# Kernel optimization log

Hardware: AMD Instinct MI355X
Metric: run time of the kernel (lower is better)

The kernel has to match this reference:

```python
import jax, jax.numpy as jnp
import numpy as np

N_HEADS = 16

def setup_inputs() -> dict:
    key = jax.random.key(0)
    ks = jax.random.split(key, 8)
    bs, t, h, dh = 32, 512, 1024, 64
    s = lambda k, shape: jax.random.normal(k, shape, dtype=jnp.float32) * 0.02
    return {
        "x": jax.random.normal(ks[0], (bs, t, h), dtype=jnp.float32),
        "Wq": s(ks[1], (h, h)),
        "bq": s(ks[2], (h,)),
        "Wk": s(ks[3], (h, h)),
        "bk": s(ks[4], (h,)),
        "Wv": s(ks[5], (h, dh)),
        "bv": s(ks[6], (dh,)),
        "Wo": s(ks[7], (dh, h)),
    }

def reference(x, Wq, bq, Wk, bk, Wv, bv, Wo):
    bs, t, h = x.shape
    dh = Wv.shape[1]
    nh = N_HEADS
    # projections (context == x; static_features=None path)
    q = (x @ Wq + bq).reshape(bs, t, nh, dh)   # [b,t,h,d]
    k = (x @ Wk + bk).reshape(bs, t, nh, dh)
    v = x @ Wv + bv                             # shared single-head V: [b,t,d]
    scale = dh ** -0.5
    # per-head scores [b,h,q,k]
    score = jnp.einsum('bqhd,bkhd->bhqk', q, k) * scale
    # causal mask (mask_future_timesteps=True): -inf above diagonal
    mask = jnp.triu(jnp.full((t, t), -jnp.inf, dtype=score.dtype), 1)
    score = score + mask
    prob = jax.nn.softmax(score, axis=-1)       # attn_dropout is identity (p=0)
    # broadcast shared V across heads
    attn_vec = jnp.einsum('bhqk,bkd->bhqd', prob, v)   # [b,h,t,d]
    m_attn_vec = jnp.mean(attn_vec, axis=1)            # head-mean pooling [b,t,d]
    out = m_attn_vec @ Wo                              # out_proj, no bias; out_dropout identity
    return out, attn_vec
```

## Files before the change

### kernel.cpp

```cpp
#include <hip/hip_runtime.h>
#include <hip/hip_bf16.h>
#include <math.h>

#define BS 32
#define TT 512
#define HH 1024
#define NH 16
#define DH 64
#define MM (BS*TT)
#define NCAT 2176

typedef __attribute__((ext_vector_type(8))) __bf16 bf16x8;
typedef __attribute__((ext_vector_type(4))) float  f32x4;

#define QSCALE 0.18033688011112042f

__device__ __forceinline__ void gld16(const void* g, void* l) {
    __builtin_amdgcn_global_load_lds(
        (const __attribute__((address_space(1))) unsigned int*)g,
        (__attribute__((address_space(3))) unsigned int*)l,
        16, 0, 0);
}

__global__ __launch_bounds__(256) void cvt_x(const float* __restrict__ x,
                                             __bf16* __restrict__ xb)
{
    const size_t i = ((size_t)blockIdx.x * 256 + threadIdx.x) * 8;
    float4 a = *(const float4*)(x + i);
    float4 b = *(const float4*)(x + i + 4);
    bf16x8 v;
    v[0] = (__bf16)a.x; v[1] = (__bf16)a.y; v[2] = (__bf16)a.z; v[3] = (__bf16)a.w;
    v[4] = (__bf16)b.x; v[5] = (__bf16)b.y; v[6] = (__bf16)b.z; v[7] = (__bf16)b.w;
    *(bf16x8*)(xb + i) = v;
}

__global__ __launch_bounds__(256) void prep_w(
    const float* __restrict__ Wq, const float* __restrict__ Wk,
    const float* __restrict__ Wv, const float* __restrict__ bq_,
    const float* __restrict__ bk_, const float* __restrict__ bv_,
    __bf16* __restrict__ Wt, float* __restrict__ bias_cat)
{
    __shared__ __align__(16) __bf16 tile[64][72];
    const int tid = threadIdx.x;
    const int n0 = blockIdx.x * 64;
    const int k0 = blockIdx.y * 64;

    const int n_l = tid & 63;
    const int k_b = tid >> 6;
    const int n   = n0 + n_l;
    #pragma unroll
    for (int j = 0; j < 16; ++j) {
        const int k_l = j * 4 + k_b;
        const int k   = k0 + k_l;
        float v;
        if (n < 1024)      v = Wq[(size_t)k * 1024 + n];
        else if (n < 2048) v = Wk[(size_t)k * 1024 + (n - 1024)];
        else if (n < 2112) v = Wv[(size_t)k * 64 + (n - 2048)];
        else               v = 0.f;
        tile[n_l][k_l] = (__bf16)v;
    }
    if (blockIdx.y == 0 && tid < 64) {
        const int nn = n0 + tid;
        bias_cat[nn] = (nn < 1024) ? bq_[nn]
                     : (nn < 2048) ? bk_[nn - 1024]
                     : (nn < 2112) ? bv_[nn - 2048] : 0.f;
    }
    __syncthreads();
    const int n_l2 = tid >> 2;
    const int k_l2 = (tid & 3) * 16;
    __bf16* dst = Wt + (size_t)(n0 + n_l2) * 1024 + k0 + k_l2;
    *(bf16x8*)dst       = *(const bf16x8*)&tile[n_l2][k_l2];
    *(bf16x8*)(dst + 8) = *(const bf16x8*)&tile[n_l2][k_l2 + 8];
}

__global__ __launch_bounds__(256) void gemm_qkv(
    const __bf16* __restrict__ A, const __bf16* __restrict__ B,
    const float* __restrict__ bias_cat,
    __bf16* __restrict__ Qo, __bf16* __restrict__ Ko,
    __bf16* __restrict__ Vt)
{
    __shared__ __align__(16) __bf16 sA[128 * 32];
    __shared__ __align__(16) __bf16 sB[128 * 32];

    const int tid  = threadIdx.x;
    const int wv   = tid >> 6;
    const int ln   = tid & 63;
    const int quad = ln >> 4;
    const int l16  = ln & 15;
    const int m0 = blockIdx.y * 128;
    const int n0 = blockIdx.x * 128;

    const int rw = (wv & 1) * 64;
    const int cw = (wv >> 1) * 64;

    f32x4 acc[4][4];
    #pragma unroll
    for (int i = 0; i < 4; ++i)
        #pragma unroll
        for (int j = 0; j < 4; ++j) acc[i][j] = f32x4{0, 0, 0, 0};

    const int srow = wv * 16 + (ln >> 2);
    const int scol = (ln & 3) * 8;
    const __bf16* ga0 = A + (size_t)(m0 + srow) * 1024 + scol;
    const __bf16* gb0 = B + (size_t)(n0 + srow) * 1024 + scol;
    __bf16* la0 = sA + wv * 512;
    __bf16* lb0 = sB + wv * 512;

    for (int k0 = 0; k0 < 1024; k0 += 32) {
        gld16(ga0 + k0, la0);
        gld16(ga0 + (size_t)64 * 1024 + k0, la0 + 2048);
        gld16(gb0 + k0, lb0);
        gld16(gb0 + (size_t)64 * 1024 + k0, lb0 + 2048);
        __syncthreads();

        bf16x8 af[4], bfr[4];
        #pragma unroll
        for (int mt = 0; mt < 4; ++mt)
            af[mt] = *(const bf16x8*)&sA[(rw + mt * 16 + l16) * 32 + quad * 8];
        #pragma unroll
        for (int nt = 0; nt < 4; ++nt)
            bfr[nt] = *(const bf16x8*)&sB[(cw + nt * 16 + l16) * 32 + quad * 8];
        #pragma unroll
        for (int mt = 0; mt < 4; ++mt)
            #pragma unroll
            for (int nt = 0; nt < 4; ++nt)
                acc[mt][nt] = __builtin_amdgcn_mfma_f32_16x16x32_bf16(af[mt], bfr[nt], acc[mt][nt], 0, 0, 0);
        __syncthreads();
    }

    #pragma unroll
    for (int mt = 0; mt < 4; ++mt) {
        #pragma unroll
        for (int nt = 0; nt < 4; ++nt) {
            const int colb = n0 + cw + nt * 16 + l16;
            if (colb >= 2112) continue;
            const float bias = bias_cat[colb];
            #pragma unroll
            for (int r = 0; r < 4; ++r) {
                const int row = m0 + rw + mt * 16 + quad * 4 + r;
                const int b = row >> 9, t = row & 511;
                float v = acc[mt][nt][r] + bias;
                if (colb < 1024) {
                    const int h = colb >> 6, d = colb & 63;
                    Qo[(((size_t)(b * NH + h) * TT) + t) * DH + d] = (__bf16)(v * QSCALE);
                } else if (colb < 2048) {
                    const int c = colb - 1024;
                    const int h = c >> 6, d = c & 63;
                    Ko[(((size_t)(b * NH + h) * TT) + t) * DH + d] = (__bf16)v;
                } else {
                    const int d = colb - 2048;
                    Vt[((size_t)(b * DH + d)) * TT + t] = (__bf16)v;
                }
            }
        }
    }
}

__global__ __launch_bounds__(1024) void attn_mfma(
    const __bf16* __restrict__ Q, const __bf16* __restrict__ K,
    const __bf16* __restrict__ Vt, float* __restrict__ attn_vec,
    float* __restrict__ mav)
{
    __shared__ float smav[64][65];

    const int wave = threadIdx.x >> 6;
    const int lane = threadIdx.x & 63;
    const int pair = blockIdx.x & 7;
    const int b    = blockIdx.x >> 3;
    const int bh   = b * NH + wave;
    const int quad = lane >> 4;
    const int l16  = lane & 15;

    {
        float* p = &smav[0][0];
        for (int i = threadIdx.x; i < 64 * 65; i += 1024) p[i] = 0.f;
    }
    __syncthreads();

    const __bf16* Qbh = Q  + (size_t)bh * TT * DH;
    const __bf16* Kbh = K  + (size_t)bh * TT * DH;
    const __bf16* Vb  = Vt + (size_t)b  * DH * TT;

    const int perm = ((l16 >> 2) << 3) + (l16 & 3);
    const __bf16* kp1 = Kbh + (size_t)perm * DH;
    const __bf16* kp2 = Kbh + (size_t)(perm + 4) * DH;

    #pragma unroll 1
    for (int rep = 0; rep < 2; ++rep) {
        const int qt2 = rep ? (15 - pair) : pair;
        const int q0  = qt2 << 5;
        const int kend = q0 + 32;

        const bf16x8 qA_lo = *(const bf16x8*)(Qbh + (size_t)(q0 + l16) * DH + quad * 8);
        const bf16x8 qA_hi = *(const bf16x8*)(Qbh + (size_t)(q0 + l16) * DH + 32 + quad * 8);
        const bf16x8 qB_lo = *(const bf16x8*)(Qbh + (size_t)(q0 + 16 + l16) * DH + quad * 8);
        const bf16x8 qB_hi = *(const bf16x8*)(Qbh + (size_t)(q0 + 16 + l16) * DH + 32 + quad * 8);

        f32x4 OA[4] = {f32x4{0,0,0,0}, f32x4{0,0,0,0}, f32x4{0,0,0,0}, f32x4{0,0,0,0}};
        f32x4 OB[4] = {f32x4{0,0,0,0}, f32x4{0,0,0,0}, f32x4{0,0,0,0}, f32x4{0,0,0,0}};
        float lA = 0.f, lB = 0.f;

        bf16x8 k1a = *(const bf16x8*)(kp1 + quad * 8);
        bf16x8 k1b = *(const bf16x8*)(kp1 + 32 + quad * 8);
        bf16x8 k2a = *(const bf16x8*)(kp2 + quad * 8);
        bf16x8 k2b = *(const bf16x8*)(kp2 + 32 + quad * 8);

        for (int kb0 = 0; kb0 < kend; kb0 += 32) {
            const __bf16* vp = Vb + (size_t)l16 * TT + kb0 + quad * 8;
            bf16x8 vf0 = *(const bf16x8*)(vp);
            bf16x8 vf1 = *(const bf16x8*)(vp + (size_t)16 * TT);
            bf16x8 vf2 = *(const bf16x8*)(vp + (size_t)32 * TT);
            bf16x8 vf3 = *(const bf16x8*)(vp + (size_t)48 * TT);

            f32x4 s1A = __builtin_amdgcn_mfma_f32_16x16x32_bf16(k1a, qA_lo, f32x4{0,0,0,0}, 0, 0, 0);
            s1A       = __builtin_amdgcn_mfma_f32_16x16x32_bf16(k1b, qA_hi, s1A, 0, 0, 0);
            f32x4 s2A = __builtin_amdgcn_mfma_f32_16x16x32_bf16(k2a, qA_lo, f32x4{0,0,0,0}, 0, 0, 0);
            s2A       = __builtin_amdgcn_mfma_f32_16x16x32_bf16(k2b, qA_hi, s2A, 0, 0, 0);
            f32x4 s1B = __builtin_amdgcn_mfma_f32_16x16x32_bf16(k1a, qB_lo, f32x4{0,0,0,0}, 0, 0, 0);
            s1B       = __builtin_amdgcn_mfma_f32_16x16x32_bf16(k1b, qB_hi, s1B, 0, 0, 0);
            f32x4 s2B = __builtin_amdgcn_mfma_f32_16x16x32_bf16(k2a, qB_lo, f32x4{0,0,0,0}, 0, 0, 0);
            s2B       = __builtin_amdgcn_mfma_f32_16x16x32_bf16(k2b, qB_hi, s2B, 0, 0, 0);

            {
                const int kbn = (kb0 + 32 < kend) ? kb0 + 32 : kb0;
                const __bf16* nk1 = kp1 + (size_t)kbn * DH;
                const __bf16* nk2 = kp2 + (size_t)kbn * DH;
                k1a = *(const bf16x8*)(nk1 + quad * 8);
                k1b = *(const bf16x8*)(nk1 + 32 + quad * 8);
                k2a = *(const bf16x8*)(nk2 + quad * 8);
                k2b = *(const bf16x8*)(nk2 + 32 + quad * 8);
            }

            if (kb0 == q0) {
                const int qqA = q0 + l16, qqB = q0 + 16 + l16;
                #pragma unroll
                for (int r = 0; r < 4; ++r) {
                    const int key1 = kb0 + quad * 8 + r;
                    const int key2 = key1 + 4;
                    if (key1 > qqA) s1A[r] = -INFINITY;
                    if (key2 > qqA) s2A[r] = -INFINITY;
                    if (key1 > qqB) s1B[r] = -INFINITY;
                    if (key2 > qqB) s2B[r] = -INFINITY;
                }
            }

            bf16x8 pfA, pfB;
            float psA = 0.f, psB = 0.f;
            #pragma unroll
            for (int r = 0; r < 4; ++r) {
                float pa0 = exp2f(s1A[r]);
                float pa1 = exp2f(s2A[r]);
                float pb0 = exp2f(s1B[r]);
                float pb1 = exp2f(s2B[r]);
                psA += pa0 + pa1;
                psB += pb0 + pb1;
                pfA[r]     = (__bf16)pa0;
                pfA[4 + r] = (__bf16)pa1;
                pfB[r]     = (__bf16)pb0;
                pfB[4 + r] = (__bf16)pb1;
            }
            lA += psA;
            lB += psB;

            OA[0] = __builtin_amdgcn_mfma_f32_16x16x32_bf16(pfA, vf0, OA[0], 0, 0, 0);
            OB[0] = __builtin_amdgcn_mfma_f32_16x16x32_bf16(pfB, vf0, OB[0], 0, 0, 0);
            OA[1] = __builtin_amdgcn_mfma_f32_16x16x32_bf16(pfA, vf1, OA[1], 0, 0, 0);
            OB[1] = __builtin_amdgcn_mfma_f32_16x16x32_bf16(pfB, vf1, OB[1], 0, 0, 0);
            OA[2] = __builtin_amdgcn_mfma_f32_16x16x32_bf16(pfA, vf2, OA[2], 0, 0, 0);
            OB[2] = __builtin_amdgcn_mfma_f32_16x16x32_bf16(pfB, vf2, OB[2], 0, 0, 0);
            OA[3] = __builtin_amdgcn_mfma_f32_16x16x32_bf16(pfA, vf3, OA[3], 0, 0, 0);
            OB[3] = __builtin_amdgcn_mfma_f32_16x16x32_bf16(pfB, vf3, OB[3], 0, 0, 0);
        }

        lA += __shfl_xor(lA, 16);
        lA += __shfl_xor(lA, 32);
        lB += __shfl_xor(lB, 16);
        lB += __shfl_xor(lB, 32);

        #pragma unroll
        for (int r = 0; r < 4; ++r) {
            const float invA = 1.0f / __shfl(lA, quad * 4 + r);
            const float invB = 1.0f / __shfl(lB, quad * 4 + r);
            const int tA = q0 + quad * 4 + r;
            const int tB = tA + 16;
            const int ltA = rep * 32 + quad * 4 + r;
            const int ltB = ltA + 16;
            float* opA = attn_vec + ((size_t)bh * TT + tA) * DH + l16;
            float* opB = attn_vec + ((size_t)bh * TT + tB) * DH + l16;
            #pragma unroll
            for (int nt = 0; nt < 4; ++nt) {
                const float vA = OA[nt][r] * invA;
                const float vB = OB[nt][r] * invB;
                opA[nt * 16] = vA;
                opB[nt * 16] = vB;
                atomicAdd(&smav[ltA][nt * 16 + l16], vA * (1.f / 16.f));
                atomicAdd(&smav[ltB][nt * 16 + l16], vB * (1.f / 16.f));
            }
        }
    }

    __syncthreads();

    {
        const int row = threadIdx.x >> 4;
        const int d0  = (threadIdx.x & 15) * 4;
        const int t   = (row < 32) ? ((pair << 5) + row)
                                   : (((15 - pair) << 5) + (row - 32));
        float4 v;
        v.x = smav[row][d0];
        v.y = smav[row][d0 + 1];
        v.z = smav[row][d0 + 2];
        v.w = smav[row][d0 + 3];
        *(float4*)(mav + ((size_t)(b * TT + t)) * DH + d0) = v;
    }
}

__global__ __launch_bounds__(256) void gemm_out(
    const float* __restrict__ A, const float* __restrict__ B,
    float* __restrict__ C, int M, int N, int K)
{
    __shared__ __align__(16) __bf16 sA[64][32];
    __shared__ __align__(16) __bf16 sB[64][32];

    const int tid  = threadIdx.x;
    const int wave = tid >> 6;
    const int lane = tid & 63;
    const int m0 = blockIdx.y * 64;
    const int n0 = blockIdx.x * 64;

    f32x4 acc[4] = {f32x4{0,0,0,0}, f32x4{0,0,0,0}, f32x4{0,0,0,0}, f32x4{0,0,0,0}};

    const int ar = tid >> 2;
    const int ac = (tid & 3) * 8;
    const int bk = tid >> 3;
    const int bc = (tid & 7) * 8;
    const int quad = lane >> 4;
    const int l16  = lane & 15;

    for (int k0 = 0; k0 < K; k0 += 32) {
        const float* ap = A + (size_t)(m0 + ar) * K + k0 + ac;
        float4 a0 = *(const float4*)ap;
        float4 a1 = *(const float4*)(ap + 4);
        {
            bf16x8 av;
            av[0] = (__bf16)a0.x; av[1] = (__bf16)a0.y; av[2] = (__bf16)a0.z; av[3] = (__bf16)a0.w;
            av[4] = (__bf16)a1.x; av[5] = (__bf16)a1.y; av[6] = (__bf16)a1.z; av[7] = (__bf16)a1.w;
            *(bf16x8*)&sA[ar][ac] = av;
        }
        const float* bp = B + (size_t)(k0 + bk) * N + n0 + bc;
        float4 b0 = *(const float4*)bp;
        float4 b1 = *(const float4*)(bp + 4);
        sB[bc + 0][bk] = (__bf16)b0.x;
        sB[bc + 1][bk] = (__bf16)b0.y;
        sB[bc + 2][bk] = (__bf16)b0.z;
        sB[bc + 3][bk] = (__bf16)b0.w;
        sB[bc + 4][bk] = (__bf16)b1.x;
        sB[bc + 5][bk] = (__bf16)b1.y;
        sB[bc + 6][bk] = (__bf16)b1.z;
        sB[bc + 7][bk] = (__bf16)b1.w;
        __syncthreads();

        bf16x8 afrag = *(const bf16x8*)&sA[wave * 16 + l16][quad * 8];
        #pragma unroll
        for (int tn = 0; tn < 4; ++tn) {
            bf16x8 bfrag = *(const bf16x8*)&sB[tn * 16 + l16][quad * 8];
            acc[tn] = __builtin_amdgcn_mfma_f32_16x16x32_bf16(afrag, bfrag, acc[tn], 0, 0, 0);
        }
        __syncthreads();
    }

    #pragma unroll
    for (int tn = 0; tn < 4; ++tn) {
        #pragma unroll
        for (int r = 0; r < 4; ++r) {
            int row = m0 + wave * 16 + quad * 4 + r;
            int col = n0 + tn * 16 + l16;
            C[(size_t)row * N + col] = acc[tn][r];
        }
    }
}

extern "C" void kernel_launch(void* const* d_in, const int* in_sizes, int n_in,
                              void* d_out, int out_size, void* d_ws, size_t ws_size,
                              hipStream_t stream)
{
    const float* x  = (const float*)d_in[0];
    const float* Wq = (const float*)d_in[1];
    const float* bq = (const float*)d_in[2];
    const float* Wk = (const float*)d_in[3];
    const float* bk = (const float*)d_in[4];
    const float* Wv = (const float*)d_in[5];
    const float* bv = (const float*)d_in[6];
    const float* Wo = (const float*)d_in[7];

    float* out      = (float*)d_out;
    float* attn_vec = out + (size_t)MM * HH;

    char* ws = (char*)d_ws;
    __bf16* xb  = (__bf16*)ws;
    __bf16* Wt  = xb + (size_t)MM * HH;
    float* bias_cat = (float*)(Wt + (size_t)NCAT * HH);
    __bf16* Qb  = (__bf16*)(bias_cat + 2304);
    __bf16* Kb  = Qb + (size_t)MM * HH;
    __bf16* Vt  = Kb + (size_t)MM * HH;
    float*  mav = (float*)xb;

    cvt_x<<<MM * HH / (256 * 8), 256, 0, stream>>>(x, xb);
    prep_w<<<dim3(NCAT / 64, HH / 64), 256, 0, stream>>>(Wq, Wk, Wv, bq, bk, bv, Wt, bias_cat);
    gemm_qkv<<<dim3(NCAT / 128, MM / 128), 256, 0, stream>>>(xb, Wt, bias_cat, Qb, Kb, Vt);
    attn_mfma<<<BS * 8, 1024, 0, stream>>>(Qb, Kb, Vt, attn_vec, mav);
    gemm_out<<<dim3(HH / 64, MM / 64), 256, 0, stream>>>(mav, Wo, out, MM, HH, DH);
}
```

Before: 436.6 us.

## Stage V in LDS, double-prefetch K, and swizzle QKV GEMM block order

The attention kernel now loads the whole per-batch transposed V tile (64x512 bf16) into shared memory once per block with global_load_lds, replacing repeated global V loads inside the key loop. The K-fragment prefetch becomes two-deep so loads are issued a full iteration earlier. Separately, the QKV GEMM remaps block indices with a swizzle meant to improve L2 locality across the 17-column grid. This costs about 66KB more LDS per block and more registers, which may limit occupancy.

```diff
diff --git a/kernel.cpp b/kernel.cpp
--- a/kernel.cpp
+++ b/kernel.cpp
@@ -87,8 +87,11 @@
     const int ln   = tid & 63;
     const int quad = ln >> 4;
     const int l16  = ln & 15;
-    const int m0 = blockIdx.y * 128;
-    const int n0 = blockIdx.x * 128;
+
+    const int orig = blockIdx.y * 17 + blockIdx.x;
+    const int swz  = (orig & 7) * 272 + (orig >> 3);
+    const int m0 = (swz / 17) * 128;
+    const int n0 = (swz % 17) * 128;
 
     const int rw = (wv & 1) * 64;
     const int cw = (wv >> 1) * 64;
@@ -161,6 +164,7 @@
     const __bf16* __restrict__ Vt, float* __restrict__ attn_vec,
     float* __restrict__ mav)
 {
+    __shared__ __align__(16) __bf16 sV[64][520];
     __shared__ float smav[64][65];
 
     const int wave = threadIdx.x >> 6;
@@ -175,15 +179,22 @@
         float* p = &smav[0][0];
         for (int i = threadIdx.x; i < 64 * 65; i += 1024) p[i] = 0.f;
     }
-    __syncthreads();
-
-    const __bf16* Qbh = Q  + (size_t)bh * TT * DH;
-    const __bf16* Kbh = K  + (size_t)bh * TT * DH;
-    const __bf16* Vb  = Vt + (size_t)b  * DH * TT;
+
+    const __bf16* Vb = Vt + (size_t)b * DH * TT;
+    #pragma unroll
+    for (int r = 0; r < 4; ++r) {
+        const int row = wave + r * 16;
+        gld16(Vb + (size_t)row * TT + lane * 8, &sV[row][0]);
+    }
+
+    const __bf16* Qbh = Q + (size_t)bh * TT * DH;
+    const __bf16* Kbh = K + (size_t)bh * TT * DH;
 
     const int perm = ((l16 >> 2) << 3) + (l16 & 3);
     const __bf16* kp1 = Kbh + (size_t)perm * DH;
     const __bf16* kp2 = Kbh + (size_t)(perm + 4) * DH;
+
+    __syncthreads();
 
     #pragma unroll 1
     for (int rep = 0; rep < 2; ++rep) {
@@ -200,36 +211,31 @@
         f32x4 OB[4] = {f32x4{0,0,0,0}, f32x4{0,0,0,0}, f32x4{0,0,0,0}, f32x4{0,0,0,0}};
         float lA = 0.f, lB = 0.f;
 
-        bf16x8 k1a = *(const bf16x8*)(kp1 + quad * 8);
-        bf16x8 k1b = *(const bf16x8*)(kp1 + 32 + quad * 8);
-        bf16x8 k2a = *(const bf16x8*)(kp2 + quad * 8);
-        bf16x8 k2b = *(const bf16x8*)(kp2 + 32 + quad * 8);
+        bf16x8 c1a = *(const bf16x8*)(kp1 + quad * 8);
+        bf16x8 c1b = *(const bf16x8*)(kp1 + 32 + quad * 8);
+        bf16x8 c2a = *(const bf16x8*)(kp2 + quad * 8);
+        bf16x8 c2b = *(const bf16x8*)(kp2 + 32 + quad * 8);
+        const int kb1 = (32 < kend) ? 32 : 0;
+        bf16x8 n1a = *(const bf16x8*)(kp1 + (size_t)kb1 * DH + quad * 8);
+        bf16x8 n1b = *(const bf16x8*)(kp1 + (size_t)kb1 * DH + 32 + quad * 8);
+        bf16x8 n2a = *(const bf16x8*)(kp2 + (size_t)kb1 * DH + quad * 8);
+        bf16x8 n2b = *(const bf16x8*)(kp2 + (size_t)kb1 * DH + 32 + quad * 8);
 
         for (int kb0 = 0; kb0 < kend; kb0 += 32) {
-            const __bf16* vp = Vb + (size_t)l16 * TT + kb0 + quad * 8;
-            bf16x8 vf0 = *(const bf16x8*)(vp);
-            bf16x8 vf1 = *(const bf16x8*)(vp + (size_t)16 * TT);
-            bf16x8 vf2 = *(const bf16x8*)(vp + (size_t)32 * TT);
-            bf16x8 vf3 = *(const bf16x8*)(vp + (size_t)48 * TT);
-
-            f32x4 s1A = __builtin_amdgcn_mfma_f32_16x16x32_bf16(k1a, qA_lo, f32x4{0,0,0,0}, 0, 0, 0);
-            s1A       = __builtin_amdgcn_mfma_f32_16x16x32_bf16(k1b, qA_hi, s1A, 0, 0, 0);
-            f32x4 s2A = __builtin_amdgcn_mfma_f32_16x16x32_bf16(k2a, qA_lo, f32x4{0,0,0,0}, 0, 0, 0);
-            s2A       = __builtin_amdgcn_mfma_f32_16x16x32_bf16(k2b, qA_hi, s2A, 0, 0, 0);
-            f32x4 s1B = __builtin_amdgcn_mfma_f32_16x16x32_bf16(k1a, qB_lo, f32x4{0,0,0,0}, 0, 0, 0);
-            s1B       = __builtin_amdgcn_mfma_f32_16x16x32_bf16(k1b, qB_hi, s1B, 0, 0, 0);
-            f32x4 s2B = __builtin_amdgcn_mfma_f32_16x16x32_bf16(k2a, qB_lo, f32x4{0,0,0,0}, 0, 0, 0);
-            s2B       = __builtin_amdgcn_mfma_f32_16x16x32_bf16(k2b, qB_hi, s2B, 0, 0, 0);
-
-            {
-                const int kbn = (kb0 + 32 < kend) ? kb0 + 32 : kb0;
-                const __bf16* nk1 = kp1 + (size_t)kbn * DH;
-                const __bf16* nk2 = kp2 + (size_t)kbn * DH;
-                k1a = *(const bf16x8*)(nk1 + quad * 8);
-                k1b = *(const bf16x8*)(nk1 + 32 + quad * 8);
-                k2a = *(const bf16x8*)(nk2 + quad * 8);
-                k2b = *(const bf16x8*)(nk2 + 32 + quad * 8);
-            }
+            const int vcol = kb0 + quad * 8;
+            bf16x8 vf0 = *(const bf16x8*)&sV[l16][vcol];
+            bf16x8 vf1 = *(const bf16x8*)&sV[16 + l16][vcol];
+            bf16x8 vf2 = *(const bf16x8*)&sV[32 + l16][vcol];
+            bf16x8 vf3 = *(const bf16x8*)&sV[48 + l16][vcol];
+
+            f32x4 s1A = __builtin_amdgcn_mfma_f32_16x16x32_bf16(c1a, qA_lo, f32x4{0,0,0,0}, 0, 0, 0);
+            s1A       = __builtin_amdgcn_mfma_f32_16x16x32_bf16(c1b, qA_hi, s1A, 0, 0, 0);
+            f32x4 s2A = __builtin_amdgcn_mfma_f32_16x16x32_bf16(c2a, qA_lo, f32x4{0,0,0,0}, 0, 0, 0);
+            s2A       = __builtin_amdgcn_mfma_f32_16x16x32_bf16(c2b, qA_hi, s2A, 0, 0, 0);
+            f32x4 s1B = __builtin_amdgcn_mfma_f32_16x16x32_bf16(c1a, qB_lo, f32x4{0,0,0,0}, 0, 0, 0);
+            s1B       = __builtin_amdgcn_mfma_f32_16x16x32_bf16(c1b, qB_hi, s1B, 0, 0, 0);
+            f32x4 s2B = __builtin_amdgcn_mfma_f32_16x16x32_bf16(c2a, qB_lo, f32x4{0,0,0,0}, 0, 0, 0);
+            s2B       = __builtin_amdgcn_mfma_f32_16x16x32_bf16(c2b, qB_hi, s2B, 0, 0, 0);
 
             if (kb0 == q0) {
                 const int qqA = q0 + l16, qqB = q0 + 16 + l16;
@@ -270,6 +276,15 @@
             OB[2] = __builtin_amdgcn_mfma_f32_16x16x32_bf16(pfB, vf2, OB[2], 0, 0, 0);
             OA[3] = __builtin_amdgcn_mfma_f32_16x16x32_bf16(pfA, vf3, OA[3], 0, 0, 0);
             OB[3] = __builtin_amdgcn_mfma_f32_16x16x32_bf16(pfB, vf3, OB[3], 0, 0, 0);
+
+            c1a = n1a; c1b = n1b; c2a = n2a; c2b = n2b;
+            const int kbn = (kb0 + 64 < kend) ? kb0 + 64 : kend - 32;
+            const __bf16* nk1 = kp1 + (size_t)kbn * DH;
+            const __bf16* nk2 = kp2 + (size_t)kbn * DH;
+            n1a = *(const bf16x8*)(nk1 + quad * 8);
+            n1b = *(const bf16x8*)(nk1 + 32 + quad * 8);
+            n2a = *(const bf16x8*)(nk2 + quad * 8);
+            n2b = *(const bf16x8*)(nk2 + 32 + quad * 8);
         }
 
         lA += __shfl_xor(lA, 16);
```

New measurement: 427.5 us. -2.1%, faster.
